# Performance work log

Hardware: AMD Instinct MI355X
Metric: run time of the kernel (lower is better)

## Reference

```python
import jax, jax.numpy as jnp
import numpy as np

N_HEAD = 16
HEAD_DIM = 64
ROPE_BASE = 10000.0


def _rope_cos_sin(T, dtype):
    # inv_freq: [HEAD_DIM/2]
    inv_freq = 1.0 / (ROPE_BASE ** (jnp.arange(0, HEAD_DIM, 2, dtype=jnp.float32) / HEAD_DIM))
    t = jnp.arange(T, dtype=jnp.float32)
    freqs = jnp.einsum('i,j->ij', t, inv_freq)          # [T, D/2]
    emb = jnp.concatenate([freqs, freqs], axis=-1)       # [T, D]
    return jnp.cos(emb).astype(dtype), jnp.sin(emb).astype(dtype)


def _rotate_half(x):
    x1, x2 = jnp.split(x, 2, axis=-1)
    return jnp.concatenate([-x2, x1], axis=-1)


def setup_inputs() -> dict:
    key = jax.random.key(0)
    k1, k2, k3, k4 = jax.random.split(key, 4)
    B, T, C = 4, 2048, N_HEAD * HEAD_DIM
    s = 1.0 / np.sqrt(C)
    return {
        'x': jax.random.normal(k1, (B, T, C), dtype=jnp.float32),
        'Wq': jax.random.normal(k2, (C, C), dtype=jnp.float32) * s,
        'Wkv': jax.random.normal(k3, (C, 2 * C), dtype=jnp.float32) * s,
        'Wc': jax.random.normal(k4, (C, C), dtype=jnp.float32) * s,
    }


def reference(x, Wq, Wkv, Wc):
    B, T, C = x.shape
    H, D = N_HEAD, HEAD_DIM

    q = x @ Wq                                   # [B,T,C]
    kv = x @ Wkv                                 # [B,T,2C]
    k, v = jnp.split(kv, 2, axis=-1)

    # [B,T,C] -> [B,H,T,D]
    def to_heads(t):
        return t.reshape(B, T, H, D).transpose(0, 2, 1, 3)
    q, k, v = to_heads(q), to_heads(k), to_heads(v)

    cos, sin = _rope_cos_sin(T, x.dtype)         # [T,D] each
    cos = cos[None, None]                        # [1,1,T,D]
    sin = sin[None, None]
    q = q * cos + _rotate_half(q) * sin
    k = k * cos + _rotate_half(k) * sin

    scale = 1.0 / np.sqrt(D)
    scores = jnp.einsum('bhqd,bhkd->bhqk', q, k) * scale   # [B,H,T,T]
    causal = jnp.tril(jnp.ones((T, T), dtype=bool))
    scores = jnp.where(causal, scores, jnp.finfo(scores.dtype).min)
    attn = jax.nn.softmax(scores, axis=-1)
    y = jnp.einsum('bhqk,bhkd->bhqd', attn, v)   # [B,H,T,D]
    y = y.transpose(0, 2, 1, 3).reshape(B, T, C)
    return y @ Wc
```

## Files before the change

kernel.cpp:

```cpp
#include <hip/hip_runtime.h>
#include <math.h>

typedef __attribute__((ext_vector_type(4))) float f32x4;
typedef __attribute__((ext_vector_type(16))) float f32x16;
typedef __attribute__((ext_vector_type(8))) short bf16x8;
typedef __attribute__((ext_vector_type(4))) unsigned short us4;

#define T_SEQ 2048
#define NH 16
#define HD 64
#define CDIM 1024

__device__ __forceinline__ unsigned short f2bf(float f) {
  unsigned int u = __float_as_uint(f);
  u += 0x7fffu + ((u >> 16) & 1u);
  return (unsigned short)(u >> 16);
}

__device__ __forceinline__ f32x16 zero16() {
  f32x16 z;
#pragma unroll
  for (int i = 0; i < 16; ++i) z[i] = 0.0f;
  return z;
}

#define GLOAD_LDS(g, l)                                                   \
  __builtin_amdgcn_global_load_lds(                                       \
      (const __attribute__((address_space(1))) unsigned int*)(g),         \
      (__attribute__((address_space(3))) unsigned int*)(l), 16, 0, 0)

__global__ __launch_bounds__(256) void cast_x_kernel(const float* __restrict__ src,
                                                     unsigned short* __restrict__ dst,
                                                     int n4) {
  int i = blockIdx.x * 256 + threadIdx.x;
  if (i >= n4) return;
  f32x4 v = reinterpret_cast<const f32x4*>(src)[i];
  us4 o;
#pragma unroll
  for (int j = 0; j < 4; ++j) o[j] = f2bf(v[j]);
  reinterpret_cast<us4*>(dst)[i] = o;
}

__global__ __launch_bounds__(256) void transpose_cast_kernel(const float* __restrict__ src,
                                                             unsigned short* __restrict__ dst,
                                                             int ldsrc, int lddst) {
  __shared__ float tile[32][33];
  int n0 = blockIdx.x * 32, k0 = blockIdx.y * 32;
  int tx = threadIdx.x, ty = threadIdx.y;
#pragma unroll
  for (int r = 0; r < 4; ++r)
    tile[ty + r * 8][tx] = src[(size_t)(k0 + ty + r * 8) * ldsrc + n0 + tx];
  __syncthreads();
#pragma unroll
  for (int r = 0; r < 4; ++r)
    dst[(size_t)(n0 + ty + r * 8) * lddst + k0 + tx] = f2bf(tile[tx][ty + r * 8]);
}

__global__ __launch_bounds__(256) void rope_table_kernel(float* __restrict__ cost,
                                                         float* __restrict__ sint) {
  int idx = blockIdx.x * 256 + threadIdx.x;
  int t = idx >> 5, j = idx & 31;
  double invf = pow(10000.0, -(double)j / 32.0);
  double ang = (double)t * invf;
  cost[idx] = (float)cos(ang);
  sint[idx] = (float)sin(ang);
}

template <int MODE>
__global__ __launch_bounds__(256) void gemm_kernel(
    const unsigned short* __restrict__ A, const unsigned short* __restrict__ Bt,
    int M, int N, int K,
    unsigned short* __restrict__ qo, unsigned short* __restrict__ ko,
    unsigned short* __restrict__ vTo, const float* __restrict__ cost,
    const float* __restrict__ sint, float* __restrict__ out) {
  __shared__ __align__(16) unsigned short As[128 * 32];
  __shared__ __align__(16) unsigned short Bs[128 * 32];
  const int tid = threadIdx.x;
  const int lane = tid & 63;
  const int wave = tid >> 6;
  const int wr = wave >> 1, wc = wave & 1;
  const int m0 = blockIdx.y * 128, n0 = blockIdx.x * 128;
  const int lrow = lane & 15, lhi = lane >> 4, lk8 = (lane >> 4) * 8;
  const int srow = lane >> 2, scol = (lane & 3) * 8;

  f32x4 zero4 = {0.f, 0.f, 0.f, 0.f};
  f32x4 acc[4][4];
#pragma unroll
  for (int mi = 0; mi < 4; ++mi)
#pragma unroll
    for (int ni = 0; ni < 4; ++ni) acc[mi][ni] = zero4;

  for (int kt = 0; kt < K; kt += 32) {
#pragma unroll
    for (int c2 = 0; c2 < 2; ++c2) {
      const int c = wave * 2 + c2;
      GLOAD_LDS(&A[(size_t)(m0 + c * 16 + srow) * K + kt + scol], &As[c * 512]);
      GLOAD_LDS(&Bt[(size_t)(n0 + c * 16 + srow) * K + kt + scol], &Bs[c * 512]);
    }
    __syncthreads();
    bf16x8 af[4], bfv[4];
#pragma unroll
    for (int i = 0; i < 4; ++i) {
      af[i] = *reinterpret_cast<const bf16x8*>(&As[(wr * 64 + i * 16 + lrow) * 32 + lk8]);
      bfv[i] = *reinterpret_cast<const bf16x8*>(&Bs[(wc * 64 + i * 16 + lrow) * 32 + lk8]);
    }
#pragma unroll
    for (int mi = 0; mi < 4; ++mi)
#pragma unroll
      for (int ni = 0; ni < 4; ++ni)
        acc[mi][ni] =
            __builtin_amdgcn_mfma_f32_16x16x32_bf16(af[mi], bfv[ni], acc[mi][ni], 0, 0, 0);
    __syncthreads();
  }

  if (MODE == 0) {
#pragma unroll
    for (int mi = 0; mi < 4; ++mi)
#pragma unroll
      for (int ni = 0; ni < 4; ++ni) {
        int n = n0 + wc * 64 + ni * 16 + lrow;
#pragma unroll
        for (int r = 0; r < 4; ++r) {
          int m = m0 + wr * 64 + mi * 16 + lhi * 4 + r;
          out[(size_t)m * N + n] = acc[mi][ni][r];
        }
      }
  } else {
#pragma unroll
    for (int mi = 0; mi < 4; ++mi) {
      int mb = m0 + wr * 64 + mi * 16 + lhi * 4;
      int b = mb >> 11, tb = mb & (T_SEQ - 1);
#pragma unroll
      for (int ni = 0; ni < 4; ++ni) {
        int n = n0 + wc * 64 + ni * 16 + lrow;
        int sec = n >> 10;
        int h = (n >> 6) & 15;
        int d = n & 63;
        int bh_ = b * NH + h;
        if (sec == 2) {
          int t64 = tb >> 6, ks = (tb >> 4) & 3, hiv = (tb >> 3) & 1, e0 = tb & 7;
          int dgrp = d >> 5, lanev = hiv * 32 + (d & 31);
          us4 pk;
#pragma unroll
          for (int r = 0; r < 4; ++r) pk[r] = f2bf(acc[mi][ni][r]);
          size_t addr =
              ((((size_t)bh_ * 32 + t64) * 2 + dgrp) * 4 + ks) * 512 + lanev * 8 + e0;
          *reinterpret_cast<us4*>(&vTo[addr]) = pk;
        } else {
          int dm = d & 31;
          float sgn = (d < 32) ? -1.0f : 1.0f;
          unsigned short* dstp = (sec == 0) ? qo : ko;
          int ks = d >> 4, hiq = (d >> 3) & 1, e = d & 7;
#pragma unroll
          for (int r = 0; r < 4; ++r) {
            int t = tb + r;
            float c = cost[t * 32 + dm], s = sint[t * 32 + dm];
            float val = acc[mi][ni][r] * c + sgn * acc[mi][ni ^ 2][r] * s;
            if (sec == 0) val *= 0.125f;
            int blk = t >> 5, lane_ = hiq * 32 + (t & 31);
            dstp[(((size_t)bh_ * 64 + blk) * 4 + ks) * 512 + lane_ * 8 + e] = f2bf(val);
          }
        }
      }
    }
  }
}

__global__ __launch_bounds__(256, 2) void attn_kernel(const unsigned short* __restrict__ qg,
                                                      const unsigned short* __restrict__ kg,
                                                      const unsigned short* __restrict__ vtg,
                                                      unsigned short* __restrict__ att) {
  __shared__ __align__(16) unsigned short P[4][32][72];
  const int tid = threadIdx.x;
  const int lane = tid & 63;
  const int w = tid >> 6;
  const int l31 = lane & 31, hi = lane >> 5;
  const int bid = (int)blockIdx.x;
  const int xcd = bid & 7, j = bid >> 3;
  const int bh = xcd * 8 + (j >> 3);
  const int p = (j & 7) * 4 + w;
  const unsigned short* qfp = qg + (size_t)bh * 131072;
  const unsigned short* kfp = kg + (size_t)bh * 131072;
  const unsigned short* vfp = vtg + (size_t)bh * 131072;
  const int b = bh >> 4, h = bh & 15;

  auto run_pos = [&](int pos) {
    const int qrow = pos * 32 + l31;
    bf16x8 qf[4];
#pragma unroll
    for (int ks = 0; ks < 4; ++ks)
      qf[ks] =
          *reinterpret_cast<const bf16x8*>(&qfp[((size_t)pos * 4 + ks) * 512 + lane * 8]);
    f32x16 oA = zero16(), oB = zero16();
    float mrun = -3.0e38f, lrun = 0.0f;
    const int myt = (pos >> 1) + 1;

    bf16x8 kA0[4], kB0[4], kA1[4], kB1[4];
#pragma unroll
    for (int ks = 0; ks < 4; ++ks) {
      kA0[ks] = *reinterpret_cast<const bf16x8*>(&kfp[(size_t)(0 + ks) * 512 + lane * 8]);
      kB0[ks] = *reinterpret_cast<const bf16x8*>(&kfp[(size_t)(4 + ks) * 512 + lane * 8]);
    }

    auto step = [&](int t, bf16x8 (&kcA)[4], bf16x8 (&kcB)[4], bf16x8 (&knA)[4],
                    bf16x8 (&knB)[4]) {
      bf16x8 vA[4], vB[4];
#pragma unroll
      for (int ks = 0; ks < 4; ++ks) {
        vA[ks] = *reinterpret_cast<const bf16x8*>(
            &vfp[((size_t)(2 * t) * 4 + ks) * 512 + lane * 8]);
        vB[ks] = *reinterpret_cast<const bf16x8*>(
            &vfp[((size_t)(2 * t + 1) * 4 + ks) * 512 + lane * 8]);
      }
      f32x16 sA = zero16(), sB = zero16();
      __builtin_amdgcn_s_setprio(1);
#pragma unroll
      for (int ks = 0; ks < 4; ++ks) {
        sA = __builtin_amdgcn_mfma_f32_32x32x16_bf16(kcA[ks], qf[ks], sA, 0, 0, 0);
        sB = __builtin_amdgcn_mfma_f32_32x32x16_bf16(kcB[ks], qf[ks], sB, 0, 0, 0);
      }
      __builtin_amdgcn_s_setprio(0);
      if (t + 1 < myt) {
#pragma unroll
        for (int ks = 0; ks < 4; ++ks) {
          knA[ks] = *reinterpret_cast<const bf16x8*>(
              &kfp[((size_t)(2 * t + 2) * 4 + ks) * 512 + lane * 8]);
          knB[ks] = *reinterpret_cast<const bf16x8*>(
              &kfp[((size_t)(2 * t + 3) * 4 + ks) * 512 + lane * 8]);
        }
      }
      if (t == myt - 1) {
        const int kvb = t * 64;
#pragma unroll
        for (int r = 0; r < 16; ++r) {
          int keyA = kvb + (r & 3) + 8 * (r >> 2) + 4 * hi;
          if (keyA > qrow) sA[r] = -1e30f;
          if (keyA + 32 > qrow) sB[r] = -1e30f;
        }
      }
      float tr[16];
#pragma unroll
      for (int i = 0; i < 16; ++i) tr[i] = fmaxf(sA[i], sB[i]);
#pragma unroll
      for (int i = 0; i < 8; ++i) tr[i] = fmaxf(tr[i], tr[i + 8]);
#pragma unroll
      for (int i = 0; i < 4; ++i) tr[i] = fmaxf(tr[i], tr[i + 4]);
      float tm = fmaxf(fmaxf(tr[0], tr[1]), fmaxf(tr[2], tr[3]));
      tm = fmaxf(tm, __shfl_xor(tm, 32));
      if (!__all(tm - mrun <= 8.0f)) {
        float mnew = fmaxf(mrun, tm);
        float alpha = __expf(mrun - mnew);
        lrun *= alpha;
#pragma unroll
        for (int i = 0; i < 16; ++i) {
          oA[i] *= alpha;
          oB[i] *= alpha;
        }
        mrun = mnew;
      }
#pragma unroll
      for (int i = 0; i < 16; ++i) {
        sA[i] = __expf(sA[i] - mrun);
        sB[i] = __expf(sB[i] - mrun);
      }
      float sr[16];
#pragma unroll
      for (int i = 0; i < 16; ++i) sr[i] = sA[i] + sB[i];
#pragma unroll
      for (int i = 0; i < 8; ++i) sr[i] += sr[i + 8];
#pragma unroll
      for (int i = 0; i < 4; ++i) sr[i] += sr[i + 4];
      float lsum = (sr[0] + sr[1]) + (sr[2] + sr[3]);
      lsum += __shfl_xor(lsum, 32);
      lrun += lsum;
#pragma unroll
      for (int g = 0; g < 4; ++g) {
        us4 pa, pb;
#pragma unroll
        for (int jj = 0; jj < 4; ++jj) {
          pa[jj] = f2bf(sA[4 * g + jj]);
          pb[jj] = f2bf(sB[4 * g + jj]);
        }
        *reinterpret_cast<us4*>(&P[w][l31][g * 8 + 4 * hi]) = pa;
        *reinterpret_cast<us4*>(&P[w][l31][32 + g * 8 + 4 * hi]) = pb;
      }
      __builtin_amdgcn_s_setprio(1);
#pragma unroll
      for (int ks = 0; ks < 4; ++ks) {
        bf16x8 pf = *reinterpret_cast<const bf16x8*>(&P[w][l31][ks * 16 + hi * 8]);
        oA = __builtin_amdgcn_mfma_f32_32x32x16_bf16(vA[ks], pf, oA, 0, 0, 0);
        oB = __builtin_amdgcn_mfma_f32_32x32x16_bf16(vB[ks], pf, oB, 0, 0, 0);
      }
      __builtin_amdgcn_s_setprio(0);
    };

    int t = 0;
    while (t < myt) {
      step(t, kA0, kB0, kA1, kB1);
      ++t;
      if (t >= myt) break;
      step(t, kA1, kB1, kA0, kB0);
      ++t;
    }

    const float inv = 1.0f / lrun;
    const size_t obase = ((size_t)b * T_SEQ + qrow) * CDIM + h * HD;
#pragma unroll
    for (int g = 0; g < 4; ++g) {
      us4 pa, pb;
#pragma unroll
      for (int jj = 0; jj < 4; ++jj) {
        pa[jj] = f2bf(oA[4 * g + jj] * inv);
        pb[jj] = f2bf(oB[4 * g + jj] * inv);
      }
      *reinterpret_cast<us4*>(&att[obase + g * 8 + 4 * hi]) = pa;
      *reinterpret_cast<us4*>(&att[obase + 32 + g * 8 + 4 * hi]) = pb;
    }
  };

  run_pos(63 - p);
  run_pos(p);
}

extern "C" void kernel_launch(void* const* d_in, const int* in_sizes, int n_in,
                              void* d_out, int out_size, void* d_ws, size_t ws_size,
                              hipStream_t stream) {
  const float* x = (const float*)d_in[0];
  const float* Wq = (const float*)d_in[1];
  const float* Wkv = (const float*)d_in[2];
  const float* Wc = (const float*)d_in[3];
  float* out = (float*)d_out;

  char* ws = (char*)d_ws;
  size_t off = 0;
  auto alloc = [&](size_t bytes) {
    void* p = ws + off;
    off += (bytes + 255) & ~(size_t)255;
    return p;
  };
  const size_t NTOK = 4ull * T_SEQ;
  const size_t NELEM = NTOK * CDIM;
  unsigned short* xb = (unsigned short*)alloc(NELEM * 2);
  unsigned short* WT = (unsigned short*)alloc(3072ull * 1024 * 2);
  unsigned short* WcT = (unsigned short*)alloc(1024ull * 1024 * 2);
  unsigned short* qb = (unsigned short*)alloc(NELEM * 2);
  unsigned short* kb = (unsigned short*)alloc(NELEM * 2);
  unsigned short* vT = (unsigned short*)alloc(NELEM * 2);
  float* cost = (float*)alloc(T_SEQ * 32 * 4);
  float* sint = (float*)alloc(T_SEQ * 32 * 4);
  unsigned short* att = xb;

  cast_x_kernel<<<(int)(NELEM / 4 / 256), 256, 0, stream>>>(x, xb, (int)(NELEM / 4));
  transpose_cast_kernel<<<dim3(32, 32), dim3(32, 8), 0, stream>>>(Wq, WT, 1024, 1024);
  transpose_cast_kernel<<<dim3(64, 32), dim3(32, 8), 0, stream>>>(Wkv, WT + 1024 * 1024, 2048,
                                                                  1024);
  transpose_cast_kernel<<<dim3(32, 32), dim3(32, 8), 0, stream>>>(Wc, WcT, 1024, 1024);
  rope_table_kernel<<<T_SEQ * 32 / 256, 256, 0, stream>>>(cost, sint);

  gemm_kernel<1><<<dim3(3072 / 128, NTOK / 128), 256, 0, stream>>>(
      xb, WT, (int)NTOK, 3072, 1024, qb, kb, vT, cost, sint, nullptr);

  attn_kernel<<<dim3(512), 256, 0, stream>>>(qb, kb, vT, att);

  gemm_kernel<0><<<dim3(1024 / 128, NTOK / 128), 256, 0, stream>>>(
      att, WcT, (int)NTOK, 1024, 1024, nullptr, nullptr, nullptr, nullptr, nullptr, out);
}
```

Measured before the change: 201.7 us.

## Add 4-stage LDS pipeline and XOR swizzle to GEMM kernel

```diff
diff --git a/kernel.cpp b/kernel.cpp
--- a/kernel.cpp
+++ b/kernel.cpp
@@ -67,21 +67,22 @@
 }
 
 template <int MODE>
-__global__ __launch_bounds__(256) void gemm_kernel(
+__global__ __launch_bounds__(256, 2) void gemm_kernel(
     const unsigned short* __restrict__ A, const unsigned short* __restrict__ Bt,
     int M, int N, int K,
     unsigned short* __restrict__ qo, unsigned short* __restrict__ ko,
     unsigned short* __restrict__ vTo, const float* __restrict__ cost,
     const float* __restrict__ sint, float* __restrict__ out) {
-  __shared__ __align__(16) unsigned short As[128 * 32];
-  __shared__ __align__(16) unsigned short Bs[128 * 32];
+  __shared__ __align__(16) unsigned short As[4][128 * 32];
+  __shared__ __align__(16) unsigned short Bs[4][128 * 32];
   const int tid = threadIdx.x;
   const int lane = tid & 63;
   const int wave = tid >> 6;
   const int wr = wave >> 1, wc = wave & 1;
   const int m0 = blockIdx.y * 128, n0 = blockIdx.x * 128;
-  const int lrow = lane & 15, lhi = lane >> 4, lk8 = (lane >> 4) * 8;
-  const int srow = lane >> 2, scol = (lane & 3) * 8;
+  const int lrow = lane & 15, lhi = lane >> 4;
+  const int srow = lane >> 2;
+  const int scol = ((lane & 3) ^ ((srow >> 1) & 3)) * 8;
 
   f32x4 zero4 = {0.f, 0.f, 0.f, 0.f};
   f32x4 acc[4][4];
@@ -90,19 +91,34 @@
 #pragma unroll
     for (int ni = 0; ni < 4; ++ni) acc[mi][ni] = zero4;
 
-  for (int kt = 0; kt < K; kt += 32) {
+  const int ntiles = K >> 5;
+  auto stage = [&](int bf, int kt) {
 #pragma unroll
     for (int c2 = 0; c2 < 2; ++c2) {
       const int c = wave * 2 + c2;
-      GLOAD_LDS(&A[(size_t)(m0 + c * 16 + srow) * K + kt + scol], &As[c * 512]);
-      GLOAD_LDS(&Bt[(size_t)(n0 + c * 16 + srow) * K + kt + scol], &Bs[c * 512]);
-    }
-    __syncthreads();
+      GLOAD_LDS(&A[(size_t)(m0 + c * 16 + srow) * K + kt + scol], &As[bf][c * 512]);
+      GLOAD_LDS(&Bt[(size_t)(n0 + c * 16 + srow) * K + kt + scol], &Bs[bf][c * 512]);
+    }
+  };
+
+  stage(0, 0);
+  stage(1, 32);
+  stage(2, 64);
+  for (int ti = 0; ti < ntiles; ++ti) {
+    asm volatile("s_waitcnt vmcnt(8)" ::: "memory");
+    __builtin_amdgcn_s_barrier();
+    __builtin_amdgcn_sched_barrier(0);
+    if (ti + 3 < ntiles) stage((ti + 3) & 3, (ti + 3) * 32);
+    const int cur = ti & 3;
     bf16x8 af[4], bfv[4];
 #pragma unroll
     for (int i = 0; i < 4; ++i) {
-      af[i] = *reinterpret_cast<const bf16x8*>(&As[(wr * 64 + i * 16 + lrow) * 32 + lk8]);
-      bfv[i] = *reinterpret_cast<const bf16x8*>(&Bs[(wc * 64 + i * 16 + lrow) * 32 + lk8]);
+      const int ra = wr * 64 + i * 16 + lrow;
+      const int rb = wc * 64 + i * 16 + lrow;
+      af[i] = *reinterpret_cast<const bf16x8*>(
+          &As[cur][ra * 32 + (lhi ^ ((ra >> 1) & 3)) * 8]);
+      bfv[i] = *reinterpret_cast<const bf16x8*>(
+          &Bs[cur][rb * 32 + (lhi ^ ((rb >> 1) & 3)) * 8]);
     }
 #pragma unroll
     for (int mi = 0; mi < 4; ++mi)
@@ -110,7 +126,6 @@
       for (int ni = 0; ni < 4; ++ni)
         acc[mi][ni] =
             __builtin_amdgcn_mfma_f32_16x16x32_bf16(af[mi], bfv[ni], acc[mi][ni], 0, 0, 0);
-    __syncthreads();
   }
 
   if (MODE == 0) {
```

Result: faster. 197.3 us (-2.2%).
